# Kernel tuning notes

Measured on AMD Instinct MI355X. Metric: run time of the kernel, lower is better.

Reference implementation:

```python
import jax, jax.numpy as jnp
import numpy as np

B, D, E, K, C = 16384, 256, 16, 4, 10
EPS = 1e-5  # torch LayerNorm default eps


def setup_inputs() -> dict:
    key = jax.random.key(0)
    ks = jax.random.split(key, 5)
    s = 0.02
    return {
        "features": jax.random.normal(ks[0], (B, D), dtype=jnp.float32),
        "router_w": jax.random.normal(ks[1], (D, E), dtype=jnp.float32) * s,
        "router_b": jnp.zeros((E,), dtype=jnp.float32),
        "ln_g": jnp.ones((E, D), dtype=jnp.float32),
        "ln_b": jnp.zeros((E, D), dtype=jnp.float32),
        "w1": jax.random.normal(ks[2], (E, D, D), dtype=jnp.float32) * s,
        "b1": jnp.zeros((E, D), dtype=jnp.float32),
        "w2": jax.random.normal(ks[3], (E, D, C), dtype=jnp.float32) * s,
        "b2": jnp.zeros((E, C), dtype=jnp.float32),
    }


def reference(features, router_w, router_b, ln_g, ln_b, w1, b1, w2, b2):
    # Router: [B,D] @ [D,E] -> [B,E]
    gate_logits = features @ router_w + router_b
    gate_probs = jax.nn.softmax(gate_logits, axis=-1)
    topk_vals, topk_idx = jax.lax.top_k(gate_probs, K)  # [B,K]
    topk_vals = topk_vals / topk_vals.sum(axis=-1, keepdims=True)

    # Shared LayerNorm statistics (per-sample), per-expert affine.
    mu = features.mean(axis=-1, keepdims=True)
    var = ((features - mu) ** 2).mean(axis=-1, keepdims=True)
    xhat = (features - mu) * jax.lax.rsqrt(var + EPS)  # [B,D]
    xn = ln_g[:, None, :] * xhat[None, :, :] + ln_b[:, None, :]  # [E,B,D]

    # All experts densely (batched GEMMs), exact (erf) GELU like torch.
    h = jax.nn.gelu(jnp.einsum('ebd,edh->ebh', xn, w1) + b1[:, None, :],
                    approximate=False)  # [E,B,D]
    all_logits_e = jnp.einsum('ebh,ehc->ebc', h, w2) + b2[:, None, :]  # [E,B,C]
    all_logits = jnp.transpose(all_logits_e, (1, 0, 2))  # [B,E,C]

    # Gather top-k experts' logits and mix their softmaxed probs.
    idx = jnp.broadcast_to(topk_idx[:, :, None], (features.shape[0], K, C))
    selected = jnp.take_along_axis(all_logits, idx, axis=1)  # [B,K,C]
    market_probs = (topk_vals[:, :, None] * jax.nn.softmax(selected, axis=-1)).sum(axis=1)

    all_probs = jax.nn.softmax(all_logits_e, axis=-1)  # [E,B,C]
    return market_probs, all_probs, gate_probs
```

## Files before the change

kernel.cpp:

```cpp
#include <hip/hip_runtime.h>
#include <hip/hip_bf16.h>
#include <stdint.h>


typedef __bf16 bf16;
typedef __bf16 bf16x8 __attribute__((ext_vector_type(8)));
typedef __bf16 bf16x4 __attribute__((ext_vector_type(4)));
typedef float  f32x4  __attribute__((ext_vector_type(4)));

#define XK_OFF   0UL
#define W1T_OFF  8388608UL
#define W2T_OFF  10485760UL
#define B1P_OFF  10616832UL
#define TKI_OFF  10633216UL
#define TKW_OFF  10895360UL

#define APROBS_OFF 163840UL
#define GATE_OFF   2785280UL

#define LOG2E 1.4426950408889634f

__device__ __forceinline__ void gl_lds16(const void* g, void* l) {
  __builtin_amdgcn_global_load_lds((const __attribute__((address_space(1))) void*)g,
                                   (__attribute__((address_space(3))) void*)l, 16, 0, 0);
}

__device__ __forceinline__ uint32_t cvt_pk_bf16(float a, float b) {
  uint32_t r;
  asm("v_cvt_pk_bf16_f32 %0, %1, %2" : "=v"(r) : "v"(a), "v"(b));
  return r;
}

__device__ __forceinline__ float gelu_f(float x) {
  float e = __builtin_amdgcn_exp2f(-2.45541f * x);
  return x * __builtin_amdgcn_rcpf(e + 1.0f);
}

__global__ __launch_bounds__(256) void k_pre(const float* __restrict__ feat,
                                             const float* __restrict__ rw,
                                             const float* __restrict__ rb,
                                             const float* __restrict__ ln_g,
                                             const float* __restrict__ ln_b,
                                             const float* __restrict__ b1,
                                             const float* __restrict__ w1,
                                             const float* __restrict__ w2,
                                             float* __restrict__ out,
                                             char* __restrict__ ws) {
  __shared__ __align__(16) char sm[20736];
  const int bid = blockIdx.x;
  const int t = threadIdx.x;

  if (bid < 256) {
    float (*tile)[68] = (float(*)[68])sm;
    const int e = bid >> 4, kt = (bid >> 2) & 3, nt = bid & 3;
    {
      const int r = t >> 2, cs = t & 3;
      const float* src = w1 + ((size_t)e * 256 + kt * 64 + r) * 256 + nt * 64 + cs * 16;
#pragma unroll
      for (int j = 0; j < 4; ++j) {
        float4 v = *(const float4*)(src + j * 4);
        *(float4*)(&tile[r][cs * 16 + j * 4]) = v;
      }
    }
    __syncthreads();
    {
      const int rn = t >> 2, ks = t & 3;
      const int n = nt * 64 + rn;
      bf16* base = (bf16*)(ws + W1T_OFF) + (size_t)e * 65536;
      float pb = 0.f;
#pragma unroll
      for (int j = 0; j < 4; ++j) {
        int kc = ks * 16 + j * 4;
        int k0 = kt * 64 + kc;
        float4 g4 = *(const float4*)(ln_g + e * 256 + k0);
        float4 l4 = *(const float4*)(ln_b + e * 256 + k0);
        float t0 = tile[kc + 0][rn], t1 = tile[kc + 1][rn];
        float t2 = tile[kc + 2][rn], t3 = tile[kc + 3][rn];
        bf16x4 o;
        o[0] = (bf16)(t0 * g4.x);
        o[1] = (bf16)(t1 * g4.y);
        o[2] = (bf16)(t2 * g4.z);
        o[3] = (bf16)(t3 * g4.w);
        pb += l4.x * t0 + l4.y * t1 + l4.z * t2 + l4.w * t3;
        *(bf16x4*)(base + (k0 >> 5) * 8192 + n * 32 + (k0 & 31)) = o;
      }
      pb += __shfl_xor(pb, 1);
      pb += __shfl_xor(pb, 2);
      if (ks == 0) {
        if (kt == 0) pb += b1[e * 256 + n];
        atomicAdd((float*)(ws + B1P_OFF) + e * 256 + n, pb);
      }
    }
  } else if (bid < 272) {
    const int e = bid - 256;
    const int c = t >> 4, hs = t & 15;
    bf16* dst = (bf16*)(ws + W2T_OFF) + (size_t)e * 4096 + c * 256 + hs * 16;
#pragma unroll
    for (int j4 = 0; j4 < 4; ++j4) {
      bf16x4 o;
#pragma unroll
      for (int j = 0; j < 4; ++j) {
        int h = hs * 16 + j4 * 4 + j;
        float v = (c < 10) ? w2[((size_t)e * 256 + h) * 10 + c] : 0.0f;
        o[j] = (bf16)v;
      }
      *(bf16x4*)(dst + j4 * 4) = o;
    }
  } else {
    float (*rwt)[260] = (float(*)[260])sm;
    float (*xrow)[256] = (float(*)[256])(sm + 16640);
    const int w = t >> 6, l = t & 63;
    const int b = (bid - 272) * 4 + w;

    float4 x4 = *(const float4*)(feat + (size_t)b * 256 + l * 4);

#pragma unroll
    for (int i = 0; i < 16; ++i) {
      int idx = t + 256 * i;
      rwt[idx & 15][idx >> 4] = rw[idx];
    }
    *(float4*)(&xrow[w][l * 4]) = x4;

    float s = x4.x + x4.y + x4.z + x4.w;
    float s2 = x4.x * x4.x + x4.y * x4.y + x4.z * x4.z + x4.w * x4.w;
#pragma unroll
    for (int off = 1; off < 64; off <<= 1) {
      s += __shfl_xor(s, off);
      s2 += __shfl_xor(s2, off);
    }
    float mu = s * (1.0f / 256.0f);
    float var = s2 * (1.0f / 256.0f) - mu * mu;
    float rstd = __builtin_amdgcn_rsqf(var + 1e-5f);
    bf16x4 hb;
    hb[0] = (bf16)((x4.x - mu) * rstd);
    hb[1] = (bf16)((x4.y - mu) * rstd);
    hb[2] = (bf16)((x4.z - mu) * rstd);
    hb[3] = (bf16)((x4.w - mu) * rstd);
    *(bf16x4*)((bf16*)(ws + XK_OFF) + ((size_t)(b >> 7) * 32768) + (l >> 3) * 4096 +
               (b & 127) * 32 + (l & 7) * 4) = hb;

    __syncthreads();

    const int e = l & 15, q = l >> 4;
    float g = 0.f;
#pragma unroll
    for (int i = 0; i < 16; ++i) {
      float4 xv = *(const float4*)(&xrow[w][q * 64 + i * 4]);
      float4 wv = *(const float4*)(&rwt[e][q * 64 + i * 4]);
      g += xv.x * wv.x + xv.y * wv.y + xv.z * wv.z + xv.w * wv.w;
    }
    g += __shfl_xor(g, 16);
    g += __shfl_xor(g, 32);
    g += rb[e];

    float m = g;
#pragma unroll
    for (int off = 1; off < 16; off <<= 1) m = fmaxf(m, __shfl_xor(m, off));
    float p = __builtin_amdgcn_exp2f((g - m) * LOG2E);
    float sum = p;
#pragma unroll
    for (int off = 1; off < 16; off <<= 1) sum += __shfl_xor(sum, off);
    float prob = p * __builtin_amdgcn_rcpf(sum);
    if (q == 0) out[GATE_OFF + (size_t)b * 16 + e] = prob;

    float pv[16];
#pragma unroll
    for (int i = 0; i < 16; ++i) pv[i] = __shfl(prob, i);
    int idxk[4];
    float valk[4];
#pragma unroll
    for (int k = 0; k < 4; ++k) {
      float best = pv[0];
      int bi = 0;
#pragma unroll
      for (int i = 1; i < 16; ++i) {
        if (pv[i] > best) { best = pv[i]; bi = i; }
      }
      valk[k] = best;
      idxk[k] = bi;
#pragma unroll
      for (int i = 0; i < 16; ++i) pv[i] = (i == bi) ? -1.0f : pv[i];
    }
    float wsum = valk[0] + valk[1] + valk[2] + valk[3];
    float rn = __builtin_amdgcn_rcpf(wsum);
    if (l == 0) {
      int4 iv = {idxk[0], idxk[1], idxk[2], idxk[3]};
      float4 wv = {valk[0] * rn, valk[1] * rn, valk[2] * rn, valk[3] * rn};
      *(int4*)(ws + TKI_OFF + (size_t)b * 16) = iv;
      *(float4*)(ws + TKW_OFF + (size_t)b * 16) = wv;
    }
  }
}

__global__ __launch_bounds__(512, 4) void k_moe(const char* __restrict__ ws,
                                                const float* __restrict__ b2g,
                                                float* __restrict__ out) {
  __shared__ __align__(16) char smem[73728];
  const int lin = blockIdx.x;
  const int e = (lin >> 3) & 15;
  const int mt = (lin & 7) * 16 + (lin >> 7);
  const int m0 = mt * 128;
  const int t = threadIdx.x;
  const int wid = t >> 6, l = t & 63;
  const int lq = l >> 4, lr = l & 15;
  const int wnb = wid >> 1;
  const int wsb = wid & 1;
  const int el = lr & 7;

  const uint16_t* xk = (const uint16_t*)(ws + XK_OFF) + (size_t)mt * 32768;
  const uint16_t* w1km = (const uint16_t*)(ws + W1T_OFF) + (size_t)e * 65536;
  const uint16_t* w2t = (const uint16_t*)(ws + W2T_OFF) + (size_t)e * 4096;
  const float* b1p = (const float*)(ws + B1P_OFF) + e * 256;

  const int pn = t >> 3, hf = (t >> 2) & 1, sl = t & 3;
  const int srcoff = (2 * pn + hf) * 32 + ((sl ^ (pn & 3)) * 8);
  const uint16_t* sW = w1km + srcoff;
  const uint16_t* sX = xk + srcoff;
  const uint16_t* sW2 = w2t + (t >> 5) * 256 + (((t & 31) ^ ((t >> 5) & 7)) * 8);

  gl_lds16(sW2, smem + 65536 + wid * 1024);
  gl_lds16(sW, smem + wid * 1024);
  gl_lds16(sW + 4096, smem + 8192 + wid * 1024);
  gl_lds16(sX, smem + 32768 + wid * 1024);

  const int pr = lr >> 1;
  const int fsw = (lr & 1) * 64 + ((lq ^ (pr & 3)) << 4);
  const int aoffb = (wnb * 32 + pr) * 128 + fsw;
  const int xoffb = (wsb * 32 + pr) * 128 + fsw;

  f32x4 zz = {0.f, 0.f, 0.f, 0.f};
  f32x4 acc[4][4];
#pragma unroll
  for (int mi = 0; mi < 4; ++mi)
#pragma unroll
    for (int nj = 0; nj < 4; ++nj) acc[mi][nj] = zz;

  __syncthreads();
#pragma unroll
  for (int kt = 0; kt < 8; ++kt) {
    const int buf = kt & 1;
    if (kt < 7) {
      const uint16_t* a = sW + (kt + 1) * 8192;
      char* dW = smem + (buf ^ 1) * 16384 + wid * 1024;
      gl_lds16(a, dW);
      gl_lds16(a + 4096, dW + 8192);
      gl_lds16(sX + (kt + 1) * 4096, smem + 32768 + (buf ^ 1) * 8192 + wid * 1024);
    }
    bf16x8 af[4], xf[4];
#pragma unroll
    for (int mi = 0; mi < 4; ++mi)
      af[mi] = *(const bf16x8*)(smem + buf * 16384 + aoffb + mi * 1024);
#pragma unroll
    for (int nj = 0; nj < 4; ++nj)
      xf[nj] = *(const bf16x8*)(smem + 32768 + buf * 8192 + xoffb + nj * 1024);
    __builtin_amdgcn_s_setprio(1);
#pragma unroll
    for (int mi = 0; mi < 4; ++mi)
#pragma unroll
      for (int nj = 0; nj < 4; ++nj)
        acc[mi][nj] = __builtin_amdgcn_mfma_f32_16x16x32_bf16(af[mi], xf[nj], acc[mi][nj], 0, 0, 0);
    __builtin_amdgcn_s_setprio(0);
    __syncthreads();
  }

  float4 bn[4];
#pragma unroll
  for (int mi = 0; mi < 4; ++mi)
    bn[mi] = *(const float4*)(b1p + wnb * 64 + mi * 16 + lq * 4);
#pragma unroll
  for (int mi = 0; mi < 4; ++mi) {
    const int nbase = wnb * 64 + mi * 16 + lq * 4;
    const int gsw = (nbase >> 3) << 4;
    const int gsub = (nbase & 7) << 1;
#pragma unroll
    for (int nj = 0; nj < 4; ++nj) {
      const int s = wsb * 64 + nj * 16 + lr;
      float g0 = gelu_f(acc[mi][nj][0] + bn[mi].x);
      float g1 = gelu_f(acc[mi][nj][1] + bn[mi].y);
      float g2 = gelu_f(acc[mi][nj][2] + bn[mi].z);
      float g3 = gelu_f(acc[mi][nj][3] + bn[mi].w);
      uint2 pk = {cvt_pk_bf16(g0, g1), cvt_pk_bf16(g2, g3)};
      int off = s * 512 + (gsw ^ ((s & 7) << 4)) + gsub;
      *(uint2*)(smem + off) = pk;
    }
  }
  __syncthreads();

  {
    f32x4 acc2 = {0.f, 0.f, 0.f, 0.f};
    const int arow = wid * 16 + lr;
#pragma unroll
    for (int kk = 0; kk < 8; ++kk) {
      bf16x8 a2 = *(const bf16x8*)(smem + arow * 512 + (((kk * 4 + lq) ^ el) << 4));
      bf16x8 b2f = *(const bf16x8*)(smem + 65536 + lr * 512 + (((lq + 4 * kk) ^ el) << 4));
      acc2 = __builtin_amdgcn_mfma_f32_16x16x32_bf16(a2, b2f, acc2, 0, 0, 0);
    }
    const int c = lr;
    float bias2 = (c < 10) ? b2g[e * 10 + c] : 0.0f;
#pragma unroll
    for (int rg = 0; rg < 4; ++rg) {
      float logit = acc2[rg] + bias2;
      float v = (c < 10) ? logit : -3.0e38f;
      float mx = v;
#pragma unroll
      for (int off = 1; off < 16; off <<= 1) mx = fmaxf(mx, __shfl_xor(mx, off));
      float ex = (c < 10) ? __builtin_amdgcn_exp2f((logit - mx) * LOG2E) : 0.0f;
      float sm = ex;
#pragma unroll
      for (int off = 1; off < 16; off <<= 1) sm += __shfl_xor(sm, off);
      if (c < 10) {
        float pr_ = ex * __builtin_amdgcn_rcpf(sm);
        size_t row = (size_t)e * 16384 + (m0 + wid * 16 + lq * 4 + rg);
        out[APROBS_OFF + row * 10 + c] = pr_;
      }
    }
  }
}

__global__ __launch_bounds__(256) void k_market(const char* __restrict__ ws,
                                                float* __restrict__ out) {
  const int b = blockIdx.x * 256 + threadIdx.x;
  int4 id = *(const int4*)(ws + TKI_OFF + (size_t)b * 16);
  float4 wv = *(const float4*)(ws + TKW_OFF + (size_t)b * 16);
  const int ids[4] = {id.x, id.y, id.z, id.w};
  const float wss[4] = {wv.x, wv.y, wv.z, wv.w};
  float m[10];
#pragma unroll
  for (int c = 0; c < 10; ++c) m[c] = 0.f;
#pragma unroll
  for (int k = 0; k < 4; ++k) {
    const float* ap = out + APROBS_OFF + ((size_t)ids[k] * 16384 + b) * 10;
#pragma unroll
    for (int c = 0; c < 10; ++c) m[c] += wss[k] * ap[c];
  }
#pragma unroll
  for (int c = 0; c < 10; ++c) out[(size_t)b * 10 + c] = m[c];
}

extern "C" void kernel_launch(void* const* d_in, const int* in_sizes, int n_in,
                              void* d_out, int out_size, void* d_ws, size_t ws_size,
                              hipStream_t stream) {
  (void)in_sizes; (void)n_in; (void)out_size; (void)ws_size;
  const float* feat = (const float*)d_in[0];
  const float* rw   = (const float*)d_in[1];
  const float* rb   = (const float*)d_in[2];
  const float* ln_g = (const float*)d_in[3];
  const float* ln_b = (const float*)d_in[4];
  const float* w1   = (const float*)d_in[5];
  const float* b1   = (const float*)d_in[6];
  const float* w2   = (const float*)d_in[7];
  const float* b2   = (const float*)d_in[8];
  float* out = (float*)d_out;
  char* ws = (char*)d_ws;

  hipMemsetAsync(ws + B1P_OFF, 0, 16384, stream);
  hipLaunchKernelGGL(k_pre, dim3(4368), dim3(256), 0, stream,
                     feat, rw, rb, ln_g, ln_b, b1, w1, w2, out, ws);
  hipLaunchKernelGGL(k_moe, dim3(2048), dim3(512), 0, stream, ws, b2, out);
  hipLaunchKernelGGL(k_market, dim3(64), dim3(256), 0, stream, ws, out);
}
```

Baseline: 81.79 us.

## Feed GELU accumulators directly into second GEMM and reduce partials via LDS

The second-layer GEMM now takes the post-GELU hidden activations straight from the first GEMM's accumulator registers as MFMA A-operands. Each wave computes partial logits over its own 64-wide hidden slice, using W2 fragments read from LDS. This removes the bf16 hidden-tile round trip through LDS and shrinks shared memory from 72KB to 56KB, which may allow more blocks per CU. The cost is a cross-wave reduction of four f32 partials through LDS, and the output row mapping changes to match.

After: 80.06 us. 2.1% less time.

```diff
diff --git a/kernel.cpp b/kernel.cpp
--- a/kernel.cpp
+++ b/kernel.cpp
@@ -195,7 +195,7 @@
 __global__ __launch_bounds__(512, 4) void k_moe(const char* __restrict__ ws,
                                                 const float* __restrict__ b2g,
                                                 float* __restrict__ out) {
-  __shared__ __align__(16) char smem[73728];
+  __shared__ __align__(16) char smem[57344];
   const int lin = blockIdx.x;
   const int e = (lin >> 3) & 15;
   const int mt = (lin & 7) * 16 + (lin >> 7);
@@ -218,7 +218,7 @@
   const uint16_t* sX = xk + srcoff;
   const uint16_t* sW2 = w2t + (t >> 5) * 256 + (((t & 31) ^ ((t >> 5) & 7)) * 8);
 
-  gl_lds16(sW2, smem + 65536 + wid * 1024);
+  gl_lds16(sW2, smem + 49152 + wid * 1024);
   gl_lds16(sW, smem + wid * 1024);
   gl_lds16(sW + 4096, smem + 8192 + wid * 1024);
   gl_lds16(sX, smem + 32768 + wid * 1024);
@@ -263,43 +263,71 @@
     __syncthreads();
   }
 
+  uint2 w2f[4];
+  {
+    const int q0 = wnb * 8 + (lq >> 1);
+    const int sub = (lq & 1) * 8;
+#pragma unroll
+    for (int mi = 0; mi < 4; ++mi) {
+      int q = q0 + mi * 2;
+      w2f[mi] = *(const uint2*)(smem + 49152 + lr * 512 + ((q ^ el) << 4) + sub);
+    }
+  }
+  uint4 ub0 = {w2f[0].x, w2f[0].y, w2f[1].x, w2f[1].y};
+  uint4 ub1 = {w2f[2].x, w2f[2].y, w2f[3].x, w2f[3].y};
+
   float4 bn[4];
 #pragma unroll
   for (int mi = 0; mi < 4; ++mi)
     bn[mi] = *(const float4*)(b1p + wnb * 64 + mi * 16 + lq * 4);
-#pragma unroll
-  for (int mi = 0; mi < 4; ++mi) {
-    const int nbase = wnb * 64 + mi * 16 + lq * 4;
-    const int gsw = (nbase >> 3) << 4;
-    const int gsub = (nbase & 7) << 1;
-#pragma unroll
-    for (int nj = 0; nj < 4; ++nj) {
-      const int s = wsb * 64 + nj * 16 + lr;
+
+  f32x4 acc2[4];
+#pragma unroll
+  for (int nj = 0; nj < 4; ++nj) {
+    uint32_t pk[8];
+#pragma unroll
+    for (int mi = 0; mi < 4; ++mi) {
       float g0 = gelu_f(acc[mi][nj][0] + bn[mi].x);
       float g1 = gelu_f(acc[mi][nj][1] + bn[mi].y);
       float g2 = gelu_f(acc[mi][nj][2] + bn[mi].z);
       float g3 = gelu_f(acc[mi][nj][3] + bn[mi].w);
-      uint2 pk = {cvt_pk_bf16(g0, g1), cvt_pk_bf16(g2, g3)};
-      int off = s * 512 + (gsw ^ ((s & 7) << 4)) + gsub;
-      *(uint2*)(smem + off) = pk;
-    }
+      pk[mi * 2] = cvt_pk_bf16(g0, g1);
+      pk[mi * 2 + 1] = cvt_pk_bf16(g2, g3);
+    }
+    uint4 ua0 = {pk[0], pk[1], pk[2], pk[3]};
+    uint4 ua1 = {pk[4], pk[5], pk[6], pk[7]};
+    f32x4 a2 = zz;
+    a2 = __builtin_amdgcn_mfma_f32_16x16x32_bf16(__builtin_bit_cast(bf16x8, ua0),
+                                                 __builtin_bit_cast(bf16x8, ub0), a2, 0, 0, 0);
+    a2 = __builtin_amdgcn_mfma_f32_16x16x32_bf16(__builtin_bit_cast(bf16x8, ua1),
+                                                 __builtin_bit_cast(bf16x8, ub1), a2, 0, 0, 0);
+    acc2[nj] = a2;
+  }
+
+  const int pswz = (lq ^ ((lr >> 1) & 3)) << 4;
+  {
+    const int pbase = 16384 + wnb * 1024 + lr * 64 + pswz;
+#pragma unroll
+    for (int nj = 0; nj < 4; ++nj)
+      *(f32x4*)(smem + pbase + (wsb * 4 + nj) * 4096) = acc2[nj];
   }
   __syncthreads();
 
   {
-    f32x4 acc2 = {0.f, 0.f, 0.f, 0.f};
-    const int arow = wid * 16 + lr;
-#pragma unroll
-    for (int kk = 0; kk < 8; ++kk) {
-      bf16x8 a2 = *(const bf16x8*)(smem + arow * 512 + (((kk * 4 + lq) ^ el) << 4));
-      bf16x8 b2f = *(const bf16x8*)(smem + 65536 + lr * 512 + (((lq + 4 * kk) ^ el) << 4));
-      acc2 = __builtin_amdgcn_mfma_f32_16x16x32_bf16(a2, b2f, acc2, 0, 0, 0);
-    }
+    const int rbase = 16384 + (wsb * 4 + wnb) * 4096 + lr * 64 + pswz;
+    f32x4 r0 = *(const f32x4*)(smem + rbase);
+    f32x4 r1 = *(const f32x4*)(smem + rbase + 1024);
+    f32x4 r2 = *(const f32x4*)(smem + rbase + 2048);
+    f32x4 r3 = *(const f32x4*)(smem + rbase + 3072);
+    f32x4 tot;
+#pragma unroll
+    for (int j = 0; j < 4; ++j) tot[j] = (r0[j] + r1[j]) + (r2[j] + r3[j]);
+
     const int c = lr;
     float bias2 = (c < 10) ? b2g[e * 10 + c] : 0.0f;
 #pragma unroll
     for (int rg = 0; rg < 4; ++rg) {
-      float logit = acc2[rg] + bias2;
+      float logit = tot[rg] + bias2;
       float v = (c < 10) ? logit : -3.0e38f;
       float mx = v;
 #pragma unroll
@@ -310,7 +338,7 @@
       for (int off = 1; off < 16; off <<= 1) sm += __shfl_xor(sm, off);
       if (c < 10) {
         float pr_ = ex * __builtin_amdgcn_rcpf(sm);
-        size_t row = (size_t)e * 16384 + (m0 + wid * 16 + lq * 4 + rg);
+        size_t row = (size_t)e * 16384 + (m0 + wsb * 64 + wnb * 16 + lq * 4 + rg);
         out[APROBS_OFF + row * 10 + c] = pr_;
       }
     }
```
